# Kernel optimization log

Measured on AMD Instinct MI355X. Metric: run time of the kernel, lower is better.

Reference implementation:

```python
import jax, jax.numpy as jnp
import numpy as np
import math

B, T, D = 2, 2048, 2048
NH, HD = 16, 128          # n_heads, head_dim (expand_factor=1)
LAMBDA_INIT = 0.8 - 0.6 * math.exp(-0.3 * 0)  # layer_depth=0 -> 0.2
EPS = float(jnp.finfo(jnp.float32).eps)


def rms_norm(x):
    return x * jax.lax.rsqrt(jnp.mean(x * x, axis=-1, keepdims=True) + EPS)


def apply_rotary(x, cos, sin):
    # x: (B,T,H,HD); cos/sin: (1,T,1,HD/2); half-split convention
    d = x.shape[-1] // 2
    x1, x2 = x[..., :d], x[..., d:]
    return jnp.concatenate([x1 * cos + x2 * sin, -x1 * sin + x2 * cos], axis=-1)


def causal_attn(q, k, v, scale):
    # q,k: (B,T,H,HD); v: (B,T,H,Dv) -> (B,T,H,Dv)
    Tq = q.shape[1]
    s = jnp.einsum('bqhd,bkhd->bhqk', q, k) * scale
    mask = jnp.tril(jnp.ones((Tq, Tq), dtype=bool))
    s = jnp.where(mask, s, -1e30)
    p = jax.nn.softmax(s, axis=-1)
    return jnp.einsum('bhqk,bkhd->bqhd', p, v)


def setup_inputs():
    key = jax.random.key(0)
    ks = jax.random.split(key, 8)
    x = jax.random.normal(ks[0], (B, T, D), jnp.float32)
    Wq = jax.random.normal(ks[1], (D, NH * HD), jnp.float32) * 0.02
    Wk = jax.random.normal(ks[2], (D, NH * HD), jnp.float32) * 0.02
    Wv = jax.random.normal(ks[3], (D, NH * HD), jnp.float32) * 0.02
    lambda_q1 = jax.random.normal(ks[4], (HD // 2,), jnp.float32) * 0.1
    lambda_k1 = jax.random.normal(ks[5], (HD // 2,), jnp.float32) * 0.1
    lambda_q2 = jax.random.normal(ks[6], (HD // 2,), jnp.float32) * 0.1
    lambda_k2 = jax.random.normal(ks[7], (HD // 2,), jnp.float32) * 0.1
    softmax_scaler = jnp.ones((1, 1, NH, 1), jnp.float32)
    return {"x": x, "Wq": Wq, "Wk": Wk, "Wv": Wv,
            "lambda_q1": lambda_q1, "lambda_k1": lambda_k1,
            "lambda_q2": lambda_q2, "lambda_k2": lambda_k2,
            "softmax_scaler": softmax_scaler}


def reference(x, Wq, Wk, Wv, lambda_q1, lambda_k1, lambda_q2, lambda_k2, softmax_scaler):
    b, t, _ = x.shape
    q = (x @ Wq).reshape(b, t, NH, HD)
    k = (x @ Wk).reshape(b, t, NH, HD)
    v = (x @ Wv).reshape(b, t, NH // 2, 2 * HD)

    # rotary tables (base 10000, dim=HD)
    inv_freq = 1.0 / (10000.0 ** (jnp.arange(0, HD, 2, dtype=jnp.float32) / HD))
    freqs = jnp.arange(t, dtype=jnp.float32)[:, None] * inv_freq[None, :]
    cos = jnp.cos(freqs)[None, :, None, :]
    sin = jnp.sin(freqs)[None, :, None, :]

    # qk-norm then RoPE
    q = apply_rotary(rms_norm(q), cos, sin)
    k = apply_rotary(rms_norm(k), cos, sin)

    k = k.reshape(b, t, 2, NH // 2, HD)
    k1, k2 = k[:, :, 0], k[:, :, 1]

    # scalable softmax: scale q by s * log(position)
    log_pos = jnp.log(jnp.arange(1, t + 1, dtype=jnp.float32)).reshape(1, t, 1, 1)
    q = softmax_scaler * log_pos * q

    q = q.reshape(b, t, 2, NH // 2, HD)
    q1, q2 = q[:, :, 0], q[:, :, 1]

    scale = 1.0 / math.sqrt(HD)  # flash-attn default: 1/sqrt(q head dim)
    y1 = causal_attn(q1, k1, v, scale)
    y2 = causal_attn(q2, k2, v, scale)

    lambda_1 = jnp.exp(jnp.sum(lambda_q1 * lambda_k1))
    lambda_2 = jnp.exp(jnp.sum(lambda_q2 * lambda_k2))
    lambda_full = lambda_1 - lambda_2 + LAMBDA_INIT

    y = (y1 - lambda_full * y2).reshape(b, t, D)
    return y
```

## Files before the change

kernel.cpp:

```cpp
#include <hip/hip_runtime.h>

typedef unsigned short u16;
typedef _Float16 f16;
typedef __attribute__((ext_vector_type(8))) _Float16 half8;
typedef __attribute__((ext_vector_type(4))) _Float16 half4;
typedef __attribute__((ext_vector_type(4))) float f32x4;

#define B_  2
#define T_  2048
#define D_  2048
#define NH_ 16
#define HD_ 128
#define QBLK 64
#define KBLK 32

#define MFMAH(a,b,c) __builtin_amdgcn_mfma_f32_16x16x32_f16((a),(b),(c),0,0,0)

__device__ __forceinline__ void gll16(void* lds, const void* g) {
  __builtin_amdgcn_global_load_lds(
      (const __attribute__((address_space(1))) unsigned int*)(size_t)(g),
      (__attribute__((address_space(3))) unsigned int*)(unsigned int)(size_t)(lds),
      16, 0, 0);
}

__global__ __launch_bounds__(256)
void cast_x_kernel(const float* __restrict__ X, f16* __restrict__ Xb) {
  size_t i = ((size_t)blockIdx.x * 256 + threadIdx.x) * 8;
  float4 v0 = *(const float4*)(X + i);
  float4 v1 = *(const float4*)(X + i + 4);
  half8 o;
  o[0] = (f16)v0.x; o[1] = (f16)v0.y; o[2] = (f16)v0.z; o[3] = (f16)v0.w;
  o[4] = (f16)v1.x; o[5] = (f16)v1.y; o[6] = (f16)v1.z; o[7] = (f16)v1.w;
  *(half8*)(Xb + i) = o;
}

__global__ __launch_bounds__(256)
void wt_kernel(const float* __restrict__ Wq, const float* __restrict__ Wk,
               const float* __restrict__ Wv, f16* __restrict__ Wt) {
  __shared__ float tile[32][33];
  const int z = blockIdx.z;
  const float* W = z == 0 ? Wq : (z == 1 ? Wk : Wv);
  f16* O = Wt + (size_t)z * (2048 * 2048);
  int k0 = blockIdx.x * 32, n0 = blockIdx.y * 32;
  int tx = threadIdx.x & 31, ty = threadIdx.x >> 5;
#pragma unroll
  for (int s = 0; s < 4; ++s)
    tile[ty + s * 8][tx] = W[(size_t)(k0 + ty + s * 8) * 2048 + n0 + tx];
  __syncthreads();
#pragma unroll
  for (int s = 0; s < 4; ++s) {
    int nrow = n0 + ty + s * 8;
    int orow = nrow;
    if (z < 2) {
      int hh = nrow >> 7, dd = nrow & 127;
      orow = (hh << 7) | ((dd & 63) << 1) | (dd >> 6);
    }
    O[(size_t)orow * 2048 + k0 + tx] = (f16)tile[tx][ty + s * 8];
  }
}

__global__ void rope_table_kernel(float* __restrict__ cosT, float* __restrict__ sinT) {
  int t = blockIdx.x, d = threadIdx.x;
  float invf = exp2f(-(float)d * (13.287712379549449f / 64.f));
  float fr = (float)t * invf;
  cosT[t * 64 + d] = cosf(fr);
  sinT[t * 64 + d] = sinf(fr);
}

__global__ void lambda_kernel(const float* __restrict__ lq1, const float* __restrict__ lk1,
                              const float* __restrict__ lq2, const float* __restrict__ lk2,
                              float* __restrict__ lam) {
  int l = threadIdx.x;
  float a = lq1[l] * lk1[l];
  float b = lq2[l] * lk2[l];
#pragma unroll
  for (int off = 1; off < 64; off <<= 1) { a += __shfl_xor(a, off); b += __shfl_xor(b, off); }
  if (l == 0) lam[0] = expf(a) - expf(b) + 0.2f;
}

__global__ __launch_bounds__(256)
void gemm_qkv_kernel(const f16* __restrict__ Xb, const f16* __restrict__ Wt,
                     const float* __restrict__ cosT, const float* __restrict__ sinT,
                     const float* __restrict__ scaler,
                     f16* __restrict__ Qp, f16* __restrict__ Kp,
                     f16* __restrict__ Vg) {
  __shared__ f16 As[2][128 * 32];
  __shared__ f16 Bs[2][128 * 32];
  __shared__ float ps[4][64];
  const int bid = blockIdx.x, z = blockIdx.y;
  const int lid = ((bid & 7) << 6) | (bid >> 3);
  const int bn = lid >> 5, bm = lid & 31;
  const f16* Bw = Wt + (size_t)z * (2048 * 2048);
  const int tid = threadIdx.x;
  const int w = tid >> 6, l = tid & 63;
  const int li = l & 15, lg = l >> 4;
  const int wr = w >> 1, wc = w & 1;

  f32x4 acc[4][4] = {};

  const int o0 = (w * 2 + 0) * 1024 + l * 16;
  const int o1 = (w * 2 + 1) * 1024 + l * 16;
  const int rA0 = o0 >> 6, rA1 = o1 >> 6;
  const int cs0 = ((o0 >> 4) & 3) ^ (rA0 & 3);
  const int cs1 = ((o1 >> 4) & 3) ^ (rA1 & 3);
  const f16* srcA0 = Xb + (size_t)(bm * 128 + rA0) * 2048 + cs0 * 8;
  const f16* srcA1 = Xb + (size_t)(bm * 128 + rA1) * 2048 + cs1 * 8;
  const f16* srcB0 = Bw + (size_t)(bn * 128 + rA0) * 2048 + cs0 * 8;
  const f16* srcB1 = Bw + (size_t)(bn * 128 + rA1) * 2048 + cs1 * 8;
  const int c0 = (w * 2 + 0) * 1024, c1 = (w * 2 + 1) * 1024;

#define GSTAGE(bi, kt)                                         \
  do {                                                         \
    gll16((char*)As[bi] + c0, srcA0 + (kt) * 32);              \
    gll16((char*)As[bi] + c1, srcA1 + (kt) * 32);              \
    gll16((char*)Bs[bi] + c0, srcB0 + (kt) * 32);              \
    gll16((char*)Bs[bi] + c1, srcB1 + (kt) * 32);              \
  } while (0)

  GSTAGE(0, 0);
  for (int kt = 0; kt < 64; ++kt) {
    const int cur = kt & 1;
    if (kt < 63) {
      GSTAGE(cur ^ 1, kt + 1);
      asm volatile("s_waitcnt vmcnt(4)" ::: "memory");
    } else {
      asm volatile("s_waitcnt vmcnt(0)" ::: "memory");
    }
    __builtin_amdgcn_s_barrier();
    half8 af[4], bfr[4];
#pragma unroll
    for (int mi = 0; mi < 4; ++mi) {
      int row = wr * 64 + mi * 16 + li;
      int ch = lg ^ (row & 3);
      af[mi] = *(const half8*)((const char*)As[cur] + row * 64 + ch * 16);
    }
#pragma unroll
    for (int ni = 0; ni < 4; ++ni) {
      int row = wc * 64 + ni * 16 + li;
      int ch = lg ^ (row & 3);
      bfr[ni] = *(const half8*)((const char*)Bs[cur] + row * 64 + ch * 16);
    }
    __builtin_amdgcn_s_setprio(1);
#pragma unroll
    for (int mi = 0; mi < 4; ++mi)
#pragma unroll
      for (int ni = 0; ni < 4; ++ni)
        acc[mi][ni] = MFMAH(af[mi], bfr[ni], acc[mi][ni]);
    __builtin_amdgcn_s_setprio(0);
    __builtin_amdgcn_s_barrier();
  }
#undef GSTAGE

  if (z == 2) {
#pragma unroll
    for (int mi = 0; mi < 4; ++mi)
#pragma unroll
      for (int ni = 0; ni < 4; ++ni) {
        int n = bn * 128 + wc * 64 + ni * 16 + li;
#pragma unroll
        for (int r = 0; r < 4; ++r) {
          int m = bm * 128 + wr * 64 + mi * 16 + lg * 4 + r;
          Vg[(size_t)m * 2048 + n] = (f16)acc[mi][ni][r];
        }
      }
    return;
  }

  float ss[4][4];
#pragma unroll
  for (int mi = 0; mi < 4; ++mi)
#pragma unroll
    for (int r = 0; r < 4; ++r) {
      float s = acc[mi][0][r] * acc[mi][0][r] + acc[mi][1][r] * acc[mi][1][r] +
                acc[mi][2][r] * acc[mi][2][r] + acc[mi][3][r] * acc[mi][3][r];
      s += __shfl_xor(s, 1);
      s += __shfl_xor(s, 2);
      s += __shfl_xor(s, 4);
      s += __shfl_xor(s, 8);
      ss[mi][r] = s;
    }
  if (li == 0) {
#pragma unroll
    for (int mi = 0; mi < 4; ++mi)
#pragma unroll
      for (int r = 0; r < 4; ++r)
        ps[w][mi * 16 + lg * 4 + r] = ss[mi][r];
  }
  __syncthreads();

  const int h = bn;
  f16* dst = z ? Kp : Qp;
  const float sch = scaler[h] * 0.08838834764831845f;
#pragma unroll
  for (int mi = 0; mi < 4; ++mi) {
#pragma unroll
    for (int r = 0; r < 4; ++r) {
      const int m = bm * 128 + wr * 64 + mi * 16 + lg * 4 + r;
      const int t = m & 2047, b = m >> 11;
      const int idx = mi * 16 + lg * 4 + r;
      const float tot = ps[wr * 2][idx] + ps[wr * 2 + 1][idx];
      const float rr = rsqrtf(tot * (1.f / 128.f) + 1.1920929e-07f);
      const float lm = z ? 1.f : sch * logf((float)(t + 1));
      f16* drow = dst + ((size_t)(b * 16 + h) * 2048 + t) * 128;
#pragma unroll
      for (int ni = 0; ni < 4; ++ni) {
        const int n = wc * 64 + ni * 16 + li;
        const int d1 = n >> 1;
        const float c = cosT[t * 64 + d1], s = sinT[t * 64 + d1];
        float v = acc[mi][ni][r] * rr;
        float vp = __shfl_xor(v, 1);
        float o = (li & 1) ? (v * c - vp * s) : (v * c + vp * s);
        o *= lm;
        drow[d1 + (li & 1) * 64] = (f16)o;
      }
    }
  }
}

__global__ __launch_bounds__(256)
void v_transpose_kernel(const f16* __restrict__ Vg, f16* __restrict__ Vt) {
  __shared__ f16 tile[32][34];
  const int bz = blockIdx.z;
  const int b = bz >> 3, hv = bz & 7;
  const int t0 = blockIdx.x * 32, dv0 = blockIdx.y * 32;
  const int tx = threadIdx.x & 31, ty = threadIdx.x >> 5;
#pragma unroll
  for (int s = 0; s < 4; ++s) {
    int t = t0 + ty + s * 8;
    tile[ty + s * 8][tx] = Vg[(size_t)(b * 2048 + t) * 2048 + hv * 256 + dv0 + tx];
  }
  __syncthreads();
#pragma unroll
  for (int s = 0; s < 4; ++s) {
    int dv = dv0 + ty + s * 8;
    Vt[((size_t)bz * 256 + dv) * 2048 + t0 + tx] = tile[tx][ty + s * 8];
  }
}

__global__ __launch_bounds__(256, 3)
void attn_kernel(const f16* __restrict__ Qp, const f16* __restrict__ Kp,
                 const f16* __restrict__ Vt,
                 f16* __restrict__ Y1, f16* __restrict__ Y2) {
  __shared__ f16 Ks[2][KBLK * 128];
  __shared__ f16 Vs[2][256 * KBLK];
  __shared__ f16 Ps[4][16 * 32];

  const int bid = blockIdx.x;
  const int lid = ((bid & 7) << 7) | (bid >> 3);
  const int qt = 31 - (lid & 31);
  const int bh = lid >> 5;
  const int b = bh >> 4, h = bh & 15;
  const int grp = h >> 3, hv = h & 7;
  const f16* QhP = Qp + (size_t)bh * (T_ * HD_);
  const f16* KhP = Kp + (size_t)bh * (T_ * HD_);
  const f16* Vh = Vt + (size_t)(b * 8 + hv) * (256 * T_);
  f16* Ybase = (grp ? Y2 : Y1) + (size_t)(b * 8 + hv) * T_ * 256;

  const int tid = threadIdx.x;
  const int w = tid >> 6, l = tid & 63;
  const int li = l & 15, lg = l >> 4;
  const int q0 = qt * QBLK + w * 16;

  int kRow[2], kCs[2], vDv[4], vCs[4];
#pragma unroll
  for (int i = 0; i < 2; ++i) {
    int o = (w * 2 + i) * 1024 + l * 16;
    kRow[i] = o >> 8;
    kCs[i] = ((o >> 4) & 15) ^ (kRow[i] & 7);
  }
#pragma unroll
  for (int i = 0; i < 4; ++i) {
    int o = (w * 4 + i) * 1024 + l * 16;
    vDv[i] = o >> 6;
    vCs[i] = ((o >> 4) & 3) ^ ((vDv[i] >> 1) & 3);
  }

#define STAGE(bi, kv0)                                                          \
  do {                                                                          \
    _Pragma("unroll")                                                           \
    for (int i = 0; i < 2; ++i)                                                 \
      gll16((char*)Ks[bi] + (w * 2 + i) * 1024,                                 \
            KhP + (size_t)((kv0) + kRow[i]) * 128 + kCs[i] * 8);                \
    _Pragma("unroll")                                                           \
    for (int i = 0; i < 4; ++i)                                                 \
      gll16((char*)Vs[bi] + (w * 4 + i) * 1024,                                 \
            Vh + (size_t)vDv[i] * T_ + (kv0) + vCs[i] * 8);                     \
  } while (0)

  const float L2E = 1.4426950408889634f;
  const half8 vone = {(f16)1.f, (f16)1.f, (f16)1.f, (f16)1.f,
                      (f16)1.f, (f16)1.f, (f16)1.f, (f16)1.f};

  STAGE(0, 0);

  half8 qf[4];
  {
    const f16* qrow = QhP + (size_t)(q0 + li) * 128;
#pragma unroll
    for (int kc = 0; kc < 4; ++kc)
      qf[kc] = *(const half8*)(qrow + kc * 32 + lg * 8);
  }
  f32x4 acc[16] = {};
  f32x4 acc_se = {};
  float m[4];
#pragma unroll
  for (int r = 0; r < 4; ++r) m[r] = -1e30f;

  const int nkv = (qt + 1) * 2;
  for (int kv = 0; kv < nkv; ++kv) {
    const int kv0 = kv * KBLK;
    const int cur = kv & 1;
    if (kv + 1 < nkv) {
      STAGE(cur ^ 1, kv0 + KBLK);
      asm volatile("s_waitcnt vmcnt(6)" ::: "memory");
    } else {
      asm volatile("s_waitcnt vmcnt(0)" ::: "memory");
    }
    __builtin_amdgcn_s_barrier();
    if (kv0 <= q0 + 15) {
      f32x4 s0 = {}, s1 = {}, s0b = {}, s1b = {};
      __builtin_amdgcn_s_setprio(1);
#pragma unroll
      for (int kc = 0; kc < 2; ++kc) {
        int ch = kc * 4 + lg;
        int off0 = li * 256 + ((ch ^ (li & 7)) * 16);
        int off1 = (li + 16) * 256 + ((ch ^ (li & 7)) * 16);
        const half8 k0 = *(const half8*)((const char*)Ks[cur] + off0);
        const half8 k1 = *(const half8*)((const char*)Ks[cur] + off1);
        s0 = MFMAH(qf[kc], k0, s0);
        s1 = MFMAH(qf[kc], k1, s1);
      }
#pragma unroll
      for (int kc = 2; kc < 4; ++kc) {
        int ch = kc * 4 + lg;
        int off0 = li * 256 + ((ch ^ (li & 7)) * 16);
        int off1 = (li + 16) * 256 + ((ch ^ (li & 7)) * 16);
        const half8 k0 = *(const half8*)((const char*)Ks[cur] + off0);
        const half8 k1 = *(const half8*)((const char*)Ks[cur] + off1);
        s0b = MFMAH(qf[kc], k0, s0b);
        s1b = MFMAH(qf[kc], k1, s1b);
      }
      __builtin_amdgcn_s_setprio(0);
      s0 += s0b; s1 += s1b;

      float v0[4], v1[4], tmx[4];
      const bool nomask = (kv0 + 31 <= q0);
#pragma unroll
      for (int r = 0; r < 4; ++r) {
        float a = s0[r], bb = s1[r];
        if (!nomask) {
          const int qr = q0 + lg * 4 + r;
          if (kv0 + li > qr) a = -1e30f;
          if (kv0 + 16 + li > qr) bb = -1e30f;
        }
        float t = fmaxf(a, bb);
        t = fmaxf(t, __shfl_xor(t, 1));
        t = fmaxf(t, __shfl_xor(t, 2));
        t = fmaxf(t, __shfl_xor(t, 4));
        t = fmaxf(t, __shfl_xor(t, 8));
        v0[r] = a; v1[r] = bb; tmx[r] = t;
      }
      int need = (tmx[0] > m[0] + 8.f) | (tmx[1] > m[1] + 8.f) |
                 (tmx[2] > m[2] + 8.f) | (tmx[3] > m[3] + 8.f);
      if (__any(need)) {
        float corr[4];
#pragma unroll
        for (int r = 0; r < 4; ++r) {
          float mn = fmaxf(m[r], tmx[r]);
          corr[r] = exp2f((m[r] - mn) * L2E);
          m[r] = mn;
        }
        acc_se[0] *= corr[0]; acc_se[1] *= corr[1];
        acc_se[2] *= corr[2]; acc_se[3] *= corr[3];
#pragma unroll
        for (int nt = 0; nt < 16; ++nt) {
          f32x4 a = acc[nt];
          a[0] *= corr[0]; a[1] *= corr[1]; a[2] *= corr[2]; a[3] *= corr[3];
          acc[nt] = a;
        }
      }
      f16* Pw = &Ps[w][0];
#pragma unroll
      for (int r = 0; r < 4; ++r) {
        float p0 = exp2f((v0[r] - m[r]) * L2E);
        float p1 = exp2f((v1[r] - m[r]) * L2E);
        const int rowA = lg * 4 + r;
        const int x = (rowA >> 1) & 3;
        Pw[rowA * 32 + (((li >> 3) ^ x) * 8) + (li & 7)] = (f16)p0;
        Pw[rowA * 32 + ((((li >> 3) | 2) ^ x) * 8) + (li & 7)] = (f16)p1;
      }
      const half8 pa = *(const half8*)(Pw + li * 32 + ((lg ^ ((li >> 1) & 3)) * 8));
      __builtin_amdgcn_s_setprio(1);
      acc_se = MFMAH(pa, vone, acc_se);
#pragma unroll
      for (int nt = 0; nt < 16; ++nt) {
        const int dv = nt * 16 + li;
        const int ch = lg ^ ((dv >> 1) & 3);
        const half8 vf = *(const half8*)((const char*)Vs[cur] + dv * 64 + ch * 16);
        acc[nt] = MFMAH(pa, vf, acc[nt]);
      }
      __builtin_amdgcn_s_setprio(0);
    }
    __builtin_amdgcn_s_barrier();
  }
  float inv[4];
#pragma unroll
  for (int r = 0; r < 4; ++r) inv[r] = 1.0f / acc_se[r];
  f16* Yout = Ybase + (size_t)(qt * QBLK) * 256;
#pragma unroll
  for (int nt = 0; nt < 16; ++nt)
#pragma unroll
    for (int r = 0; r < 4; ++r)
      Yout[(size_t)(w * 16 + lg * 4 + r) * 256 + nt * 16 + li] =
          (f16)(acc[nt][r] * inv[r]);
#undef STAGE
}

__global__ __launch_bounds__(256)
void combine_kernel(const f16* __restrict__ Y1, const f16* __restrict__ Y2,
                    const float* __restrict__ lamp, float* __restrict__ out) {
  size_t f = ((size_t)blockIdx.x * 256 + threadIdx.x) * 8;
  int dv = (int)(f & 255);
  int hv = (int)((f >> 8) & 7);
  size_t bt = f >> 11;
  int t = (int)(bt & 2047);
  int b = (int)(bt >> 11);
  const float lam = lamp[0];
  size_t yi = ((size_t)(b * 8 + hv) * 2048 + t) * 256 + dv;
  half8 a = *(const half8*)(Y1 + yi);
  half8 c = *(const half8*)(Y2 + yi);
  float4 o0, o1;
  o0.x = (float)a[0] - lam * (float)c[0];
  o0.y = (float)a[1] - lam * (float)c[1];
  o0.z = (float)a[2] - lam * (float)c[2];
  o0.w = (float)a[3] - lam * (float)c[3];
  o1.x = (float)a[4] - lam * (float)c[4];
  o1.y = (float)a[5] - lam * (float)c[5];
  o1.z = (float)a[6] - lam * (float)c[6];
  o1.w = (float)a[7] - lam * (float)c[7];
  *(float4*)(out + f) = o0;
  *(float4*)(out + f + 4) = o1;
}

extern "C" void kernel_launch(void* const* d_in, const int* in_sizes, int n_in,
                              void* d_out, int out_size, void* d_ws, size_t ws_size,
                              hipStream_t stream) {
  const float* x   = (const float*)d_in[0];
  const float* Wq  = (const float*)d_in[1];
  const float* Wk  = (const float*)d_in[2];
  const float* Wv  = (const float*)d_in[3];
  const float* lq1 = (const float*)d_in[4];
  const float* lk1 = (const float*)d_in[5];
  const float* lq2 = (const float*)d_in[6];
  const float* lk2 = (const float*)d_in[7];
  const float* scl = (const float*)d_in[8];
  float* out = (float*)d_out;

  char* ws = (char*)d_ws;
  f16*  Xb  = (f16*)(ws + 0);
  f16*  Wt  = (f16*)(ws + 16777216);
  f16*  Qp  = (f16*)(ws + 41943040);
  f16*  Kp  = (f16*)(ws + 58720256);
  f16*  Vg  = (f16*)(ws + 75497472);
  f16*  Vt  = (f16*)(ws + 92274688);
  f16*  Y1  = (f16*)(ws + 109051904);
  f16*  Y2  = (f16*)(ws + 125829120);
  float* cosT = (float*)(ws + 142606336);
  float* sinT = (float*)(ws + 143130624);
  float* lam  = (float*)(ws + 143654912);

  cast_x_kernel<<<4096, 256, 0, stream>>>(x, Xb);
  wt_kernel<<<dim3(64, 64, 3), 256, 0, stream>>>(Wq, Wk, Wv, Wt);
  rope_table_kernel<<<2048, 64, 0, stream>>>(cosT, sinT);
  lambda_kernel<<<1, 64, 0, stream>>>(lq1, lk1, lq2, lk2, lam);
  gemm_qkv_kernel<<<dim3(512, 3), 256, 0, stream>>>(Xb, Wt, cosT, sinT, scl, Qp, Kp, Vg);
  v_transpose_kernel<<<dim3(64, 8, 16), 256, 0, stream>>>(Vg, Vt);
  attn_kernel<<<1024, 256, 0, stream>>>(Qp, Kp, Vt, Y1, Y2);
  combine_kernel<<<4096, 256, 0, stream>>>(Y1, Y2, lam, out);
}
```

Measured before the change: 351.8 us.

## Load K tiles straight into registers with one-step prefetch instead of LDS

Drops the K shared-memory double buffer and its async global-to-LDS copy. Each wave now reads its K fragments for QK^T directly from global memory into registers and prefetches the next block's K after the score MFMAs. The wait count is adjusted so only the V copy stays in flight. This removes LDS traffic and the swizzle address math for K, but all four waves now fetch the same K tile from global/L2. It also adds 32 VGPRs per thread under a 3-blocks-per-CU launch bound and puts global latency directly on the MFMA operands.

```diff
diff --git a/kernel.cpp b/kernel.cpp
--- a/kernel.cpp
+++ b/kernel.cpp
@@ -241,7 +241,6 @@
 void attn_kernel(const f16* __restrict__ Qp, const f16* __restrict__ Kp,
                  const f16* __restrict__ Vt,
                  f16* __restrict__ Y1, f16* __restrict__ Y2) {
-  __shared__ f16 Ks[2][KBLK * 128];
   __shared__ f16 Vs[2][256 * KBLK];
   __shared__ f16 Ps[4][16 * 32];
 
@@ -261,13 +260,7 @@
   const int li = l & 15, lg = l >> 4;
   const int q0 = qt * QBLK + w * 16;
 
-  int kRow[2], kCs[2], vDv[4], vCs[4];
-#pragma unroll
-  for (int i = 0; i < 2; ++i) {
-    int o = (w * 2 + i) * 1024 + l * 16;
-    kRow[i] = o >> 8;
-    kCs[i] = ((o >> 4) & 15) ^ (kRow[i] & 7);
-  }
+  int vDv[4], vCs[4];
 #pragma unroll
   for (int i = 0; i < 4; ++i) {
     int o = (w * 4 + i) * 1024 + l * 16;
@@ -277,16 +270,23 @@
 
 #define STAGE(bi, kv0)                                                          \
   do {                                                                          \
-    _Pragma("unroll")                                                           \
-    for (int i = 0; i < 2; ++i)                                                 \
-      gll16((char*)Ks[bi] + (w * 2 + i) * 1024,                                 \
-            KhP + (size_t)((kv0) + kRow[i]) * 128 + kCs[i] * 8);                \
     _Pragma("unroll")                                                           \
     for (int i = 0; i < 4; ++i)                                                 \
       gll16((char*)Vs[bi] + (w * 4 + i) * 1024,                                 \
             Vh + (size_t)vDv[i] * T_ + (kv0) + vCs[i] * 8);                     \
   } while (0)
 
+#define KLOAD(kv0)                                                              \
+  do {                                                                          \
+    const f16* kr0 = KhP + (size_t)((kv0) + li) * 128 + lg * 8;                 \
+    const f16* kr1 = KhP + (size_t)((kv0) + 16 + li) * 128 + lg * 8;            \
+    _Pragma("unroll")                                                           \
+    for (int kc = 0; kc < 4; ++kc) {                                            \
+      kf0[kc] = *(const half8*)(kr0 + kc * 32);                                 \
+      kf1[kc] = *(const half8*)(kr1 + kc * 32);                                 \
+    }                                                                           \
+  } while (0)
+
   const float L2E = 1.4426950408889634f;
   const half8 vone = {(f16)1.f, (f16)1.f, (f16)1.f, (f16)1.f,
                       (f16)1.f, (f16)1.f, (f16)1.f, (f16)1.f};
@@ -300,6 +300,9 @@
     for (int kc = 0; kc < 4; ++kc)
       qf[kc] = *(const half8*)(qrow + kc * 32 + lg * 8);
   }
+  half8 kf0[4], kf1[4];
+  KLOAD(0);
+
   f32x4 acc[16] = {};
   f32x4 acc_se = {};
   float m[4];
@@ -312,37 +315,24 @@
     const int cur = kv & 1;
     if (kv + 1 < nkv) {
       STAGE(cur ^ 1, kv0 + KBLK);
-      asm volatile("s_waitcnt vmcnt(6)" ::: "memory");
+      asm volatile("s_waitcnt vmcnt(4)" ::: "memory");
     } else {
       asm volatile("s_waitcnt vmcnt(0)" ::: "memory");
     }
     __builtin_amdgcn_s_barrier();
-    if (kv0 <= q0 + 15) {
-      f32x4 s0 = {}, s1 = {}, s0b = {}, s1b = {};
+    const bool active = (kv0 <= q0 + 15);
+    f32x4 s0 = {}, s1 = {};
+    if (active) {
       __builtin_amdgcn_s_setprio(1);
 #pragma unroll
-      for (int kc = 0; kc < 2; ++kc) {
-        int ch = kc * 4 + lg;
-        int off0 = li * 256 + ((ch ^ (li & 7)) * 16);
-        int off1 = (li + 16) * 256 + ((ch ^ (li & 7)) * 16);
-        const half8 k0 = *(const half8*)((const char*)Ks[cur] + off0);
-        const half8 k1 = *(const half8*)((const char*)Ks[cur] + off1);
-        s0 = MFMAH(qf[kc], k0, s0);
-        s1 = MFMAH(qf[kc], k1, s1);
-      }
-#pragma unroll
-      for (int kc = 2; kc < 4; ++kc) {
-        int ch = kc * 4 + lg;
-        int off0 = li * 256 + ((ch ^ (li & 7)) * 16);
-        int off1 = (li + 16) * 256 + ((ch ^ (li & 7)) * 16);
-        const half8 k0 = *(const half8*)((const char*)Ks[cur] + off0);
-        const half8 k1 = *(const half8*)((const char*)Ks[cur] + off1);
-        s0b = MFMAH(qf[kc], k0, s0b);
-        s1b = MFMAH(qf[kc], k1, s1b);
+      for (int kc = 0; kc < 4; ++kc) {
+        s0 = MFMAH(qf[kc], kf0[kc], s0);
+        s1 = MFMAH(qf[kc], kf1[kc], s1);
       }
       __builtin_amdgcn_s_setprio(0);
-      s0 += s0b; s1 += s1b;
-
+    }
+    if (kv + 1 < nkv) KLOAD(kv0 + KBLK);
+    if (active) {
       float v0[4], v1[4], tmx[4];
       const bool nomask = (kv0 + 31 <= q0);
 #pragma unroll
@@ -414,6 +404,7 @@
       Yout[(size_t)(w * 16 + lg * 4 + r) * 256 + nt * 16 + li] =
           (f16)(acc[nt][r] * inv[r]);
 #undef STAGE
+#undef KLOAD
 }
 
 __global__ __launch_bounds__(256)
```

Measured after the change: 411.5 us. 1.17x slower.

## Split PV accumulation across waves by value columns with shared P tile

Applied to the files above, without the earlier changes.

Each wave previously ran the full 16x256 PV product for its own 16 query rows, reading all V columns from LDS. Now the softmax probabilities of all four waves go into a shared 64x32 P tile. Each wave computes a 64-row by 64-column slice of the output, loading only its 4 V fragments and reusing them across the row groups. Row rescale factors and per-wave need flags pass through LDS. This adds an extra barrier per KV step and a final shared-memory exchange of the softmax denominators, and lowers the occupancy hint from 3 to 2 blocks.

```diff
diff --git a/kernel.cpp b/kernel.cpp
--- a/kernel.cpp
+++ b/kernel.cpp
@@ -237,13 +237,16 @@
   }
 }
 
-__global__ __launch_bounds__(256, 3)
+__global__ __launch_bounds__(256, 2)
 void attn_kernel(const f16* __restrict__ Qp, const f16* __restrict__ Kp,
                  const f16* __restrict__ Vt,
                  f16* __restrict__ Y1, f16* __restrict__ Y2) {
   __shared__ f16 Ks[2][KBLK * 128];
   __shared__ f16 Vs[2][256 * KBLK];
-  __shared__ f16 Ps[4][16 * 32];
+  __shared__ f16 P_s[64 * 32];
+  __shared__ float corr_s[64];
+  __shared__ float se_s[64];
+  __shared__ unsigned flg4;
 
   const int bid = blockIdx.x;
   const int lid = ((bid & 7) << 7) | (bid >> 3);
@@ -317,7 +320,9 @@
       asm volatile("s_waitcnt vmcnt(0)" ::: "memory");
     }
     __builtin_amdgcn_s_barrier();
-    if (kv0 <= q0 + 15) {
+
+    const bool active = (kv0 <= q0 + 15);
+    if (active) {
       f32x4 s0 = {}, s1 = {}, s0b = {}, s1b = {};
       __builtin_amdgcn_s_setprio(1);
 #pragma unroll
@@ -362,8 +367,9 @@
       }
       int need = (tmx[0] > m[0] + 8.f) | (tmx[1] > m[1] + 8.f) |
                  (tmx[2] > m[2] + 8.f) | (tmx[3] > m[3] + 8.f);
-      if (__any(need)) {
-        float corr[4];
+      int na = __any(need) ? 1 : 0;
+      float corr[4] = {1.f, 1.f, 1.f, 1.f};
+      if (na) {
 #pragma unroll
         for (int r = 0; r < 4; ++r) {
           float mn = fmaxf(m[r], tmx[r]);
@@ -372,47 +378,90 @@
         }
         acc_se[0] *= corr[0]; acc_se[1] *= corr[1];
         acc_se[2] *= corr[2]; acc_se[3] *= corr[3];
-#pragma unroll
-        for (int nt = 0; nt < 16; ++nt) {
-          f32x4 a = acc[nt];
-          a[0] *= corr[0]; a[1] *= corr[1]; a[2] *= corr[2]; a[3] *= corr[3];
-          acc[nt] = a;
-        }
-      }
-      f16* Pw = &Ps[w][0];
+      }
 #pragma unroll
       for (int r = 0; r < 4; ++r) {
         float p0 = exp2f((v0[r] - m[r]) * L2E);
         float p1 = exp2f((v1[r] - m[r]) * L2E);
-        const int rowA = lg * 4 + r;
+        const int rowA = w * 16 + lg * 4 + r;
         const int x = (rowA >> 1) & 3;
-        Pw[rowA * 32 + (((li >> 3) ^ x) * 8) + (li & 7)] = (f16)p0;
-        Pw[rowA * 32 + ((((li >> 3) | 2) ^ x) * 8) + (li & 7)] = (f16)p1;
-      }
-      const half8 pa = *(const half8*)(Pw + li * 32 + ((lg ^ ((li >> 1) & 3)) * 8));
+        P_s[rowA * 32 + (((li >> 3) ^ x) * 8) + (li & 7)] = (f16)p0;
+        P_s[rowA * 32 + ((((li >> 3) | 2) ^ x) * 8) + (li & 7)] = (f16)p1;
+      }
+      if (li == 0) {
+#pragma unroll
+        for (int r = 0; r < 4; ++r) corr_s[w * 16 + lg * 4 + r] = corr[r];
+      }
+      if (l == 0) ((volatile unsigned char*)&flg4)[w] = (unsigned char)na;
+    }
+    asm volatile("s_waitcnt lgkmcnt(0)" ::: "memory");
+    __builtin_amdgcn_s_barrier();
+
+    {
+      const int dd = kv0 - qt * QBLK;
+      const int gmin = dd > 0 ? (dd >> 4) : 0;
+      unsigned fl = *(volatile unsigned*)&flg4;
+      fl &= (0xFFFFFFFFu << (gmin * 8));
+      if (fl) {
+#pragma unroll
+        for (int g = 0; g < 4; ++g) {
+          if (g >= gmin) {
+#pragma unroll
+            for (int r = 0; r < 4; ++r) {
+              const float c = corr_s[g * 16 + lg * 4 + r];
+#pragma unroll
+              for (int d = 0; d < 4; ++d) acc[g * 4 + d][r] *= c;
+            }
+          }
+        }
+      }
+      half8 vf[4];
+#pragma unroll
+      for (int d = 0; d < 4; ++d) {
+        const int dv = w * 64 + d * 16 + li;
+        const int ch = lg ^ ((dv >> 1) & 3);
+        vf[d] = *(const half8*)((const char*)Vs[cur] + dv * 64 + ch * 16);
+      }
       __builtin_amdgcn_s_setprio(1);
-      acc_se = MFMAH(pa, vone, acc_se);
-#pragma unroll
-      for (int nt = 0; nt < 16; ++nt) {
-        const int dv = nt * 16 + li;
-        const int ch = lg ^ ((dv >> 1) & 3);
-        const half8 vf = *(const half8*)((const char*)Vs[cur] + dv * 64 + ch * 16);
-        acc[nt] = MFMAH(pa, vf, acc[nt]);
+      if (active) {
+        const half8 paw = *(const half8*)((const char*)P_s +
+            (w * 16 + li) * 64 + ((lg ^ ((li >> 1) & 3)) << 4));
+        acc_se = MFMAH(paw, vone, acc_se);
+      }
+#pragma unroll
+      for (int g = 0; g < 4; ++g) {
+        if (g >= gmin) {
+          const half8 pag = *(const half8*)((const char*)P_s +
+              (g * 16 + li) * 64 + ((lg ^ ((li >> 1) & 3)) << 4));
+#pragma unroll
+          for (int d = 0; d < 4; ++d)
+            acc[g * 4 + d] = MFMAH(pag, vf[d], acc[g * 4 + d]);
+        }
       }
       __builtin_amdgcn_s_setprio(0);
     }
     __builtin_amdgcn_s_barrier();
   }
-  float inv[4];
-#pragma unroll
-  for (int r = 0; r < 4; ++r) inv[r] = 1.0f / acc_se[r];
+
+  if (li == 0) {
+#pragma unroll
+    for (int r = 0; r < 4; ++r) se_s[w * 16 + lg * 4 + r] = acc_se[r];
+  }
+  asm volatile("s_waitcnt lgkmcnt(0)" ::: "memory");
+  __builtin_amdgcn_s_barrier();
   f16* Yout = Ybase + (size_t)(qt * QBLK) * 256;
 #pragma unroll
-  for (int nt = 0; nt < 16; ++nt)
-#pragma unroll
-    for (int r = 0; r < 4; ++r)
-      Yout[(size_t)(w * 16 + lg * 4 + r) * 256 + nt * 16 + li] =
-          (f16)(acc[nt][r] * inv[r]);
+  for (int g = 0; g < 4; ++g) {
+#pragma unroll
+    for (int r = 0; r < 4; ++r) {
+      const int row = g * 16 + lg * 4 + r;
+      const float inv = 1.0f / se_s[row];
+#pragma unroll
+      for (int d = 0; d < 4; ++d)
+        Yout[(size_t)row * 256 + w * 64 + d * 16 + li] =
+            (f16)(acc[g * 4 + d][r] * inv);
+    }
+  }
 #undef STAGE
 }
 
```

Result: slower. 409.3 us (+16.3%).
